# Optimization experiments

Measured on AMD Instinct MI355X. Metric: run time of the kernel, lower is better.

Reference implementation:

```python
import jax, jax.numpy as jnp
import numpy as np

N_NODES = 250000


def _gat_conv(x, src, dst, W, att_src, att_dst, bias, n_nodes):
    # PyG GATConv, heads=1, concat=True, negative_slope=0.2, self-loops already appended.
    h = x @ W                              # [N, 2]
    a_s = h @ att_src                      # [N]
    a_d = h @ att_dst                      # [N]
    e = jax.nn.leaky_relu(a_s[src] + a_d[dst], 0.2)   # [E]
    # segment softmax over incoming edges of each dst node
    m = jax.ops.segment_max(e, dst, num_segments=n_nodes)
    e = jnp.exp(e - m[dst])
    denom = jax.ops.segment_sum(e, dst, num_segments=n_nodes)
    alpha = e / (denom[dst] + 1e-16)       # [E]
    out = jax.ops.segment_sum(alpha[:, None] * h[src], dst, num_segments=n_nodes)
    return out + bias


def setup_inputs() -> dict:
    key = jax.random.key(0)
    ks = jax.random.split(key, 10)
    N, E = N_NODES, 16000000
    x = jax.random.normal(ks[0], (N, 4), dtype=jnp.float32)
    edge_index = jax.random.randint(ks[1], (2, E), 0, N, dtype=jnp.int64)
    def gat_params(k):
        k1, k2, k3 = jax.random.split(k, 3)
        return (jax.random.normal(k1, (2, 2), dtype=jnp.float32),
                jax.random.normal(k2, (2,), dtype=jnp.float32),
                jax.random.normal(k3, (2,), dtype=jnp.float32),
                jnp.zeros((2,), dtype=jnp.float32))
    W1, as1, ad1, b1 = gat_params(ks[2])
    W2, as2, ad2, b2 = gat_params(ks[3])
    return {"x": x, "edge_index": edge_index,
            "W_F1": W1, "att_src_F1": as1, "att_dst_F1": ad1, "bias_F1": b1,
            "W_F2": W2, "att_src_F2": as2, "att_dst_F2": ad2, "bias_F2": b2}


def reference(x, edge_index, W_F1, att_src_F1, att_dst_F1, bias_F1,
              W_F2, att_src_F2, att_dst_F2, bias_F2):
    n = x.shape[0]
    loop = jnp.arange(n, dtype=edge_index.dtype)
    src = jnp.concatenate([edge_index[0], loop])
    dst = jnp.concatenate([edge_index[1], loop])
    x1, x2 = x[:, :2], x[:, 2:]
    s_x = _gat_conv(x1, src, dst, W_F1, att_src_F1, att_dst_F1, bias_F1, n)
    t_x = _gat_conv(x1, src, dst, W_F2, att_src_F2, att_dst_F2, bias_F2, n)
    x1_new = x2 * jnp.exp(s_x) + t_x
    log_det = jnp.sum(s_x, axis=1)
    return (x1_new, x2, log_det)
```

## Files before the change

### kernel.cpp

```cpp
#include <hip/hip_runtime.h>


#define BSH 8
#define BSZ 256
#define NB  977
#define CAP 17408
#define EPB 32768
#define P1T 1024
#define P2T 1024
#define MPT 17

typedef int  iv4 __attribute__((ext_vector_type(4)));
typedef _Float16 h4 __attribute__((ext_vector_type(4)));

static __device__ __forceinline__ float lrelu(float z) { return z > 0.f ? z : 0.2f * z; }

__global__ void __launch_bounds__(P1T) bin_kernel(
    const int* __restrict__ ei, int E,
    const float* __restrict__ x, int N,
    const float* __restrict__ W1, const float* __restrict__ as1, const float* __restrict__ ad1,
    const float* __restrict__ W2, const float* __restrict__ as2, const float* __restrict__ ad2,
    h4* __restrict__ nodeSh, float4* __restrict__ nodeD,
    unsigned* __restrict__ bins, unsigned* __restrict__ cursor)
{
    __shared__ unsigned sorted[EPB];
    __shared__ unsigned lhist[NB];
    __shared__ unsigned lbase[NB];
    __shared__ unsigned sbase[NB + 1];
    __shared__ unsigned swv[16];

    int tid = threadIdx.x;

    {
        int i = blockIdx.x * 512 + (tid & 511);
        if (tid < 512 && i < N) {
            float4 xv = ((const float4*)x)[i];
            float x0 = xv.x, x1v = xv.y;
            float cs1_0 = W1[0] * as1[0] + W1[1] * as1[1];
            float cs1_1 = W1[2] * as1[0] + W1[3] * as1[1];
            float cd1_0 = W1[0] * ad1[0] + W1[1] * ad1[1];
            float cd1_1 = W1[2] * ad1[0] + W1[3] * ad1[1];
            float cs2_0 = W2[0] * as2[0] + W2[1] * as2[1];
            float cs2_1 = W2[2] * as2[0] + W2[3] * as2[1];
            float cd2_0 = W2[0] * ad2[0] + W2[1] * ad2[1];
            float cd2_1 = W2[2] * ad2[0] + W2[3] * ad2[1];
            nodeSh[i] = (h4){ (_Float16)x0, (_Float16)x1v,
                              (_Float16)(x0 * cs1_0 + x1v * cs1_1),
                              (_Float16)(x0 * cs2_0 + x1v * cs2_1) };
            nodeD[i] = make_float4(x0 * cd1_0 + x1v * cd1_1, x0 * cd2_0 + x1v * cd2_1,
                                   xv.z, xv.w);
        }
    }

    for (int i = tid; i < NB; i += P1T) lhist[i] = 0u;
    __syncthreads();

    const iv4* s4 = (const iv4*)ei;
    const iv4* d4 = (const iv4*)(ei + E);
    long long vbase = ((long long)blockIdx.x * EPB) >> 2;

    iv4 dv[8];
#pragma unroll
    for (int j = 0; j < 8; ++j) {
        long long v = vbase + (long long)j * P1T + tid;
        if (v * 4 < (long long)E) dv[j] = __builtin_nontemporal_load(&d4[v]);
        else dv[j] = (iv4){-1, -1, -1, -1};
    }
    unsigned rkp[16];
#pragma unroll
    for (int j = 0; j < 8; ++j) {
        int dd[4] = { dv[j].x, dv[j].y, dv[j].z, dv[j].w };
#pragma unroll
        for (int k = 0; k < 4; ++k) {
            unsigned r = 0;
            if (dd[k] >= 0) r = atomicAdd(&lhist[((unsigned)dd[k]) >> BSH], 1u);
            int idx = j * 4 + k;
            if (idx & 1) rkp[idx >> 1] |= (r << 16);
            else         rkp[idx >> 1] = r;
        }
    }
    __syncthreads();

    {
        unsigned v = (tid < NB) ? lhist[tid] : 0u;
        unsigned lane = (unsigned)tid & 63u;
        unsigned inc = v;
#pragma unroll
        for (int off = 1; off < 64; off <<= 1) {
            unsigned u = __shfl_up(inc, off, 64);
            if (lane >= (unsigned)off) inc += u;
        }
        if (lane == 63u) swv[tid >> 6] = inc;
        __syncthreads();
        if (tid == 0) {
            unsigned s = 0;
            sbase[0] = 0;
#pragma unroll
            for (int w = 0; w < 16; ++w) { unsigned t = swv[w]; swv[w] = s; s += t; }
        }
        __syncthreads();
        if (tid < NB) {
            sbase[tid + 1] = inc + swv[tid >> 6];
            unsigned c = lhist[tid];
            if (c) lbase[tid] = (unsigned)tid * CAP + atomicAdd(&cursor[tid], c);
        }
    }
    __syncthreads();

    iv4 sv[8];
#pragma unroll
    for (int j = 0; j < 8; ++j) {
        long long v = vbase + (long long)j * P1T + tid;
        if (v * 4 < (long long)E) sv[j] = __builtin_nontemporal_load(&s4[v]);
        else sv[j] = (iv4){0, 0, 0, 0};
    }
#pragma unroll
    for (int j = 0; j < 8; ++j) {
        int ss[4] = { sv[j].x, sv[j].y, sv[j].z, sv[j].w };
        int dd[4] = { dv[j].x, dv[j].y, dv[j].z, dv[j].w };
#pragma unroll
        for (int k = 0; k < 4; ++k) {
            if (dd[k] >= 0) {
                unsigned b = ((unsigned)dd[k]) >> BSH;
                int idx = j * 4 + k;
                unsigned r = (idx & 1) ? (rkp[idx >> 1] >> 16) : (rkp[idx >> 1] & 0xFFFFu);
                sorted[sbase[b] + r] = ((unsigned)ss[k] << BSH) | ((unsigned)dd[k] & (BSZ - 1u));
            }
        }
    }
    __syncthreads();

    int wid = tid >> 6;
    unsigned lane = (unsigned)tid & 63u;
    for (int b = wid; b < NB; b += 16) {
        unsigned L  = lhist[b];
        unsigned gb = lbase[b];
        unsigned sb = sbase[b];
        unsigned room = ((unsigned)b + 1u) * CAP - gb;
        if (L > room) L = room;
        for (unsigned off = lane; off < L; off += 64u)
            bins[gb + off] = sorted[sb + off];
    }
}

__global__ void __launch_bounds__(P2T) reduce_kernel(
    const unsigned* __restrict__ bins, const unsigned* __restrict__ cursor,
    const h4* __restrict__ nodeSh, const float4* __restrict__ nodeD, int N,
    const float* __restrict__ W1, const float* __restrict__ b1,
    const float* __restrict__ W2, const float* __restrict__ b2,
    float* __restrict__ out)
{
    __shared__ unsigned sorted[CAP];
    __shared__ unsigned hist[BSZ];
    __shared__ unsigned sbase[BSZ + 1];
    __shared__ unsigned swv[BSZ / 64];
    __shared__ float4   sD[BSZ];

    int b = blockIdx.x, tid = threadIdx.x;
    int node0 = b << BSH;
    unsigned start = (unsigned)b * CAP;
    unsigned cnt = cursor[b];
    if (cnt > CAP) cnt = CAP;

    if (tid < BSZ) {
        hist[tid] = 0u;
        int n = node0 + tid;
        sD[tid] = (n < N) ? nodeD[n] : make_float4(0.f, 0.f, 0.f, 0.f);
    }
    __syncthreads();

    unsigned ev[MPT];
#pragma unroll
    for (int j = 0; j < MPT; ++j) {
        unsigned i = (unsigned)tid + (unsigned)j * P2T;
        ev[j] = (i < cnt) ? __builtin_nontemporal_load(&bins[start + i]) : 0xFFFFFFFFu;
    }
    unsigned rkp[(MPT + 1) / 2];
#pragma unroll
    for (int j = 0; j < MPT; ++j) {
        unsigned r = 0;
        if (ev[j] != 0xFFFFFFFFu) r = atomicAdd(&hist[ev[j] & (BSZ - 1u)], 1u);
        if (j & 1) rkp[j >> 1] |= (r << 16);
        else       rkp[j >> 1] = r;
    }
    __syncthreads();

    if (tid < BSZ) {
        unsigned v = hist[tid];
        unsigned lane = (unsigned)tid & 63u;
#pragma unroll
        for (int off = 1; off < 64; off <<= 1) {
            unsigned u = __shfl_up(v, off, 64);
            if (lane >= (unsigned)off) v += u;
        }
        if (lane == 63u) swv[tid >> 6] = v;
        sbase[tid + 1] = v;
    }
    __syncthreads();
    if (tid == 0) {
        unsigned s = 0;
        sbase[0] = 0;
#pragma unroll
        for (int w = 0; w < BSZ / 64; ++w) { unsigned t = swv[w]; swv[w] = s; s += t; }
    }
    __syncthreads();
    if (tid < BSZ) sbase[tid + 1] += swv[tid >> 6];
    __syncthreads();

#pragma unroll
    for (int j = 0; j < MPT; ++j) {
        if (ev[j] != 0xFFFFFFFFu) {
            unsigned r = (j & 1) ? (rkp[j >> 1] >> 16) : (rkp[j >> 1] & 0xFFFFu);
            sorted[sbase[ev[j] & (BSZ - 1u)] + r] = ev[j];
        }
    }
    __syncthreads();

    int ln = tid >> 2;
    int q  = tid & 3;
    int n = node0 + ln;
    float4 Dv = sD[ln];
    float a0 = 0.f, a1 = 0.f, a2 = 0.f, a3 = 0.f, a4 = 0.f, a5 = 0.f;
    if (n < N) {
        unsigned beg = sbase[ln], end = sbase[ln + 1];
        unsigned i = beg + (unsigned)q;
        for (; i + 12u < end; i += 16u) {
            unsigned e0 = sorted[i];
            unsigned e1 = sorted[i + 4u];
            unsigned e2 = sorted[i + 8u];
            unsigned e3 = sorted[i + 12u];
            h4 S0 = nodeSh[e0 >> BSH];
            h4 S1 = nodeSh[e1 >> BSH];
            h4 S2 = nodeSh[e2 >> BSH];
            h4 S3 = nodeSh[e3 >> BSH];
            float w;
            w = __expf(lrelu((float)S0.z + Dv.x)); a0 += w * (float)S0.x; a1 += w * (float)S0.y; a2 += w;
            w = __expf(lrelu((float)S0.w + Dv.y)); a3 += w * (float)S0.x; a4 += w * (float)S0.y; a5 += w;
            w = __expf(lrelu((float)S1.z + Dv.x)); a0 += w * (float)S1.x; a1 += w * (float)S1.y; a2 += w;
            w = __expf(lrelu((float)S1.w + Dv.y)); a3 += w * (float)S1.x; a4 += w * (float)S1.y; a5 += w;
            w = __expf(lrelu((float)S2.z + Dv.x)); a0 += w * (float)S2.x; a1 += w * (float)S2.y; a2 += w;
            w = __expf(lrelu((float)S2.w + Dv.y)); a3 += w * (float)S2.x; a4 += w * (float)S2.y; a5 += w;
            w = __expf(lrelu((float)S3.z + Dv.x)); a0 += w * (float)S3.x; a1 += w * (float)S3.y; a2 += w;
            w = __expf(lrelu((float)S3.w + Dv.y)); a3 += w * (float)S3.x; a4 += w * (float)S3.y; a5 += w;
        }
        for (; i < end; i += 4u) {
            unsigned e = sorted[i];
            h4 S = nodeSh[e >> BSH];
            float w1 = __expf(lrelu((float)S.z + Dv.x));
            float w2 = __expf(lrelu((float)S.w + Dv.y));
            float sx = (float)S.x, sy = (float)S.y;
            a0 += w1 * sx; a1 += w1 * sy; a2 += w1;
            a3 += w2 * sx; a4 += w2 * sy; a5 += w2;
        }
    }
    a0 += __shfl_xor(a0, 1); a0 += __shfl_xor(a0, 2);
    a1 += __shfl_xor(a1, 1); a1 += __shfl_xor(a1, 2);
    a2 += __shfl_xor(a2, 1); a2 += __shfl_xor(a2, 2);
    a3 += __shfl_xor(a3, 1); a3 += __shfl_xor(a3, 2);
    a4 += __shfl_xor(a4, 1); a4 += __shfl_xor(a4, 2);
    a5 += __shfl_xor(a5, 1); a5 += __shfl_xor(a5, 2);
    if (q == 0 && n < N) {
        h4 S = nodeSh[n];
        float w1s = __expf(lrelu((float)S.z + Dv.x));
        float w2s = __expf(lrelu((float)S.w + Dv.y));
        float n1x = a0 + w1s * (float)S.x;
        float n1y = a1 + w1s * (float)S.y;
        float d1  = a2 + w1s + 1e-16f;
        float n2x = a3 + w2s * (float)S.x;
        float n2y = a4 + w2s * (float)S.y;
        float d2  = a5 + w2s + 1e-16f;
        float inv1 = 1.0f / d1, inv2 = 1.0f / d2;
        float s0 = (n1x * W1[0] + n1y * W1[2]) * inv1 + b1[0];
        float s1 = (n1x * W1[1] + n1y * W1[3]) * inv1 + b1[1];
        float t0 = (n2x * W2[0] + n2y * W2[2]) * inv2 + b2[0];
        float t1 = (n2x * W2[1] + n2y * W2[3]) * inv2 + b2[1];
        float x2a = Dv.z, x2b = Dv.w;
        out[2 * n]             = x2a * __expf(s0) + t0;
        out[2 * n + 1]         = x2b * __expf(s1) + t1;
        out[2 * N + 2 * n]     = x2a;
        out[2 * N + 2 * n + 1] = x2b;
        out[4 * N + n]         = s0 + s1;
    }
}

__global__ void __launch_bounds__(256) prep_kernel(
    const float* __restrict__ x, int N,
    const float* __restrict__ W1, const float* __restrict__ as1, const float* __restrict__ ad1,
    const float* __restrict__ W2, const float* __restrict__ as2, const float* __restrict__ ad2,
    h4* __restrict__ nodeSh, float4* __restrict__ nodeD, float* __restrict__ acc)
{
    int i = blockIdx.x * blockDim.x + threadIdx.x;
    if (i >= N) return;
    float4 xv = ((const float4*)x)[i];
    float x0 = xv.x, x1v = xv.y;
    float cs1_0 = W1[0] * as1[0] + W1[1] * as1[1];
    float cs1_1 = W1[2] * as1[0] + W1[3] * as1[1];
    float cd1_0 = W1[0] * ad1[0] + W1[1] * ad1[1];
    float cd1_1 = W1[2] * ad1[0] + W1[3] * ad1[1];
    float cs2_0 = W2[0] * as2[0] + W2[1] * as2[1];
    float cs2_1 = W2[2] * as2[0] + W2[3] * as2[1];
    float cd2_0 = W2[0] * ad2[0] + W2[1] * ad2[1];
    float cd2_1 = W2[2] * ad2[0] + W2[3] * ad2[1];
    nodeSh[i] = (h4){ (_Float16)x0, (_Float16)x1v,
                      (_Float16)(x0 * cs1_0 + x1v * cs1_1),
                      (_Float16)(x0 * cs2_0 + x1v * cs2_1) };
    nodeD[i] = make_float4(x0 * cd1_0 + x1v * cd1_1, x0 * cd2_0 + x1v * cd2_1, xv.z, xv.w);
    acc[i] = 0.f; acc[N + i] = 0.f; acc[2 * N + i] = 0.f;
    acc[3 * N + i] = 0.f; acc[4 * N + i] = 0.f; acc[5 * N + i] = 0.f;
}

__global__ void __launch_bounds__(256) edge_kernel(
    const int* __restrict__ ei, int E, int N,
    const h4* __restrict__ nodeSh, const float4* __restrict__ nodeD,
    float* __restrict__ acc)
{
    int e = blockIdx.x * blockDim.x + threadIdx.x;
    if (e >= E) return;
    int s = ei[e];
    int d = ei[E + e];
    h4 S = nodeSh[s];
    float4 D = nodeD[d];
    float w1 = __expf(lrelu((float)S.z + D.x));
    float w2 = __expf(lrelu((float)S.w + D.y));
    unsafeAtomicAdd(&acc[d],         w1 * (float)S.x);
    unsafeAtomicAdd(&acc[N + d],     w1 * (float)S.y);
    unsafeAtomicAdd(&acc[2 * N + d], w1);
    unsafeAtomicAdd(&acc[3 * N + d], w2 * (float)S.x);
    unsafeAtomicAdd(&acc[4 * N + d], w2 * (float)S.y);
    unsafeAtomicAdd(&acc[5 * N + d], w2);
}

__global__ void __launch_bounds__(256) fin_kernel(
    int N,
    const float* __restrict__ W1, const float* __restrict__ b1,
    const float* __restrict__ W2, const float* __restrict__ b2,
    const h4* __restrict__ nodeSh, const float4* __restrict__ nodeD,
    const float* __restrict__ acc, float* __restrict__ out)
{
    int i = blockIdx.x * blockDim.x + threadIdx.x;
    if (i >= N) return;
    h4 S = nodeSh[i];
    float4 D = nodeD[i];
    float w1s = __expf(lrelu((float)S.z + D.x));
    float w2s = __expf(lrelu((float)S.w + D.y));
    float n1x = acc[i] + w1s * (float)S.x;
    float n1y = acc[N + i] + w1s * (float)S.y;
    float d1  = acc[2 * N + i] + w1s + 1e-16f;
    float n2x = acc[3 * N + i] + w2s * (float)S.x;
    float n2y = acc[4 * N + i] + w2s * (float)S.y;
    float d2  = acc[5 * N + i] + w2s + 1e-16f;
    float inv1 = 1.0f / d1, inv2 = 1.0f / d2;
    float s0 = (n1x * W1[0] + n1y * W1[2]) * inv1 + b1[0];
    float s1 = (n1x * W1[1] + n1y * W1[3]) * inv1 + b1[1];
    float t0 = (n2x * W2[0] + n2y * W2[2]) * inv2 + b2[0];
    float t1 = (n2x * W2[1] + n2y * W2[3]) * inv2 + b2[1];
    float x2a = D.z, x2b = D.w;
    out[2 * i]             = x2a * __expf(s0) + t0;
    out[2 * i + 1]         = x2b * __expf(s1) + t1;
    out[2 * N + 2 * i]     = x2a;
    out[2 * N + 2 * i + 1] = x2b;
    out[4 * N + i]         = s0 + s1;
}

extern "C" void kernel_launch(void* const* d_in, const int* in_sizes, int n_in,
                              void* d_out, int out_size, void* d_ws, size_t ws_size,
                              hipStream_t stream)
{
    const float* x   = (const float*)d_in[0];
    const int*   ei  = (const int*)d_in[1];
    const float* W1  = (const float*)d_in[2];
    const float* as1 = (const float*)d_in[3];
    const float* ad1 = (const float*)d_in[4];
    const float* b1  = (const float*)d_in[5];
    const float* W2  = (const float*)d_in[6];
    const float* as2 = (const float*)d_in[7];
    const float* ad2 = (const float*)d_in[8];
    const float* b2  = (const float*)d_in[9];

    int N = in_sizes[0] / 4;
    int E = in_sizes[1] / 2;

    char* ws = (char*)d_ws;
    h4*       nodeSh = (h4*)ws;
    float4*   nodeD  = (float4*)(ws + (size_t)8 * N);
    size_t    off_c  = ((size_t)24 * N + 255) & ~(size_t)255;
    unsigned* cursor = (unsigned*)(ws + off_c);
    size_t    off_b  = (off_c + 4 * NB + 255) & ~(size_t)255;
    unsigned* bins   = (unsigned*)(ws + off_b);
    float*    acc    = (float*)(ws + off_b);
    float*    out    = (float*)d_out;

    size_t need = off_b + (size_t)4 * NB * CAP;
    int gb = (E + EPB - 1) / EPB;

    if (ws_size >= need && (E % 4) == 0 && (size_t)gb * 512 >= (size_t)N) {
        hipMemsetAsync(cursor, 0, sizeof(unsigned) * NB, stream);
        bin_kernel<<<gb, P1T, 0, stream>>>(ei, E, x, N, W1, as1, ad1, W2, as2, ad2,
                                           nodeSh, nodeD, bins, cursor);
        reduce_kernel<<<NB, P2T, 0, stream>>>(bins, cursor, nodeSh, nodeD, N,
                                              W1, b1, W2, b2, out);
    } else {
        int nb = (N + 255) / 256;
        prep_kernel<<<nb, 256, 0, stream>>>(x, N, W1, as1, ad1, W2, as2, ad2,
                                            nodeSh, nodeD, acc);
        int eb = (E + 255) / 256;
        edge_kernel<<<eb, 256, 0, stream>>>(ei, E, N, nodeSh, nodeD, acc);
        fin_kernel<<<nb, 256, 0, stream>>>(N, W1, b1, W2, b2, nodeSh, nodeD, acc, out);
    }
}
```

Before: 316.2 us.

## Pack bin cursors into 64-bit atomics, hoist src loads, vectorize bin reads

```diff
diff --git a/kernel.cpp b/kernel.cpp
--- a/kernel.cpp
+++ b/kernel.cpp
@@ -4,6 +4,7 @@
 #define BSH 8
 #define BSZ 256
 #define NB  977
+#define NBP4 245
 #define CAP 17408
 #define EPB 32768
 #define P1T 1024
@@ -21,7 +22,7 @@
     const float* __restrict__ W1, const float* __restrict__ as1, const float* __restrict__ ad1,
     const float* __restrict__ W2, const float* __restrict__ as2, const float* __restrict__ ad2,
     h4* __restrict__ nodeSh, float4* __restrict__ nodeD,
-    unsigned* __restrict__ bins, unsigned* __restrict__ cursor)
+    unsigned* __restrict__ bins, unsigned long long* __restrict__ cursor)
 {
     __shared__ unsigned sorted[EPB];
     __shared__ unsigned lhist[NB];
@@ -59,13 +60,20 @@
     const iv4* d4 = (const iv4*)(ei + E);
     long long vbase = ((long long)blockIdx.x * EPB) >> 2;
 
-    iv4 dv[8];
+    iv4 dv[8], sv[8];
 #pragma unroll
     for (int j = 0; j < 8; ++j) {
         long long v = vbase + (long long)j * P1T + tid;
         if (v * 4 < (long long)E) dv[j] = __builtin_nontemporal_load(&d4[v]);
         else dv[j] = (iv4){-1, -1, -1, -1};
     }
+#pragma unroll
+    for (int j = 0; j < 8; ++j) {
+        long long v = vbase + (long long)j * P1T + tid;
+        if (v * 4 < (long long)E) sv[j] = __builtin_nontemporal_load(&s4[v]);
+        else sv[j] = (iv4){0, 0, 0, 0};
+    }
+
     unsigned rkp[16];
 #pragma unroll
     for (int j = 0; j < 8; ++j) {
@@ -99,21 +107,27 @@
             for (int w = 0; w < 16; ++w) { unsigned t = swv[w]; swv[w] = s; s += t; }
         }
         __syncthreads();
-        if (tid < NB) {
-            sbase[tid + 1] = inc + swv[tid >> 6];
-            unsigned c = lhist[tid];
-            if (c) lbase[tid] = (unsigned)tid * CAP + atomicAdd(&cursor[tid], c);
-        }
-    }
-    __syncthreads();
-
-    iv4 sv[8];
-#pragma unroll
-    for (int j = 0; j < 8; ++j) {
-        long long v = vbase + (long long)j * P1T + tid;
-        if (v * 4 < (long long)E) sv[j] = __builtin_nontemporal_load(&s4[v]);
-        else sv[j] = (iv4){0, 0, 0, 0};
-    }
+        if (tid < NB) sbase[tid + 1] = inc + swv[tid >> 6];
+        if (tid < NBP4) {
+            int b0 = tid * 4;
+            unsigned long long add = 0;
+#pragma unroll
+            for (int k = 0; k < 4; ++k) {
+                int bb = b0 + k;
+                unsigned c = (bb < NB) ? lhist[bb] : 0u;
+                add |= (unsigned long long)(c & 0xFFFFu) << (16 * k);
+            }
+            unsigned long long old = atomicAdd(&cursor[tid], add);
+#pragma unroll
+            for (int k = 0; k < 4; ++k) {
+                int bb = b0 + k;
+                if (bb < NB)
+                    lbase[bb] = (unsigned)bb * CAP + (unsigned)((old >> (16 * k)) & 0xFFFFu);
+            }
+        }
+    }
+    __syncthreads();
+
 #pragma unroll
     for (int j = 0; j < 8; ++j) {
         int ss[4] = { sv[j].x, sv[j].y, sv[j].z, sv[j].w };
@@ -144,7 +158,7 @@
 }
 
 __global__ void __launch_bounds__(P2T) reduce_kernel(
-    const unsigned* __restrict__ bins, const unsigned* __restrict__ cursor,
+    const unsigned* __restrict__ bins, const unsigned long long* __restrict__ cursor,
     const h4* __restrict__ nodeSh, const float4* __restrict__ nodeD, int N,
     const float* __restrict__ W1, const float* __restrict__ b1,
     const float* __restrict__ W2, const float* __restrict__ b2,
@@ -159,7 +173,7 @@
     int b = blockIdx.x, tid = threadIdx.x;
     int node0 = b << BSH;
     unsigned start = (unsigned)b * CAP;
-    unsigned cnt = cursor[b];
+    unsigned cnt = ((const unsigned short*)cursor)[b];
     if (cnt > CAP) cnt = CAP;
 
     if (tid < BSZ) {
@@ -170,10 +184,24 @@
     __syncthreads();
 
     unsigned ev[MPT];
-#pragma unroll
-    for (int j = 0; j < MPT; ++j) {
-        unsigned i = (unsigned)tid + (unsigned)j * P2T;
-        ev[j] = (i < cnt) ? __builtin_nontemporal_load(&bins[start + i]) : 0xFFFFFFFFu;
+    {
+        const iv4* b4 = (const iv4*)(bins + start);
+#pragma unroll
+        for (int j = 0; j < 4; ++j) {
+            unsigned g = (unsigned)tid + (unsigned)j * P2T;
+            unsigned p = 4u * g;
+            if (p + 3u < cnt) {
+                iv4 v = __builtin_nontemporal_load(&b4[g]);
+                ev[4 * j + 0] = (unsigned)v.x; ev[4 * j + 1] = (unsigned)v.y;
+                ev[4 * j + 2] = (unsigned)v.z; ev[4 * j + 3] = (unsigned)v.w;
+            } else {
+#pragma unroll
+                for (int k = 0; k < 4; ++k)
+                    ev[4 * j + k] = (p + (unsigned)k < cnt) ? bins[start + p + k] : 0xFFFFFFFFu;
+            }
+        }
+        unsigned p = 16u * P2T + (unsigned)tid;
+        ev[16] = (p < cnt) ? bins[start + p] : 0xFFFFFFFFu;
     }
     unsigned rkp[(MPT + 1) / 2];
 #pragma unroll
@@ -384,8 +412,8 @@
     h4*       nodeSh = (h4*)ws;
     float4*   nodeD  = (float4*)(ws + (size_t)8 * N);
     size_t    off_c  = ((size_t)24 * N + 255) & ~(size_t)255;
-    unsigned* cursor = (unsigned*)(ws + off_c);
-    size_t    off_b  = (off_c + 4 * NB + 255) & ~(size_t)255;
+    unsigned long long* cursor = (unsigned long long*)(ws + off_c);
+    size_t    off_b  = (off_c + 8 * NBP4 + 255) & ~(size_t)255;
     unsigned* bins   = (unsigned*)(ws + off_b);
     float*    acc    = (float*)(ws + off_b);
     float*    out    = (float*)d_out;
@@ -394,7 +422,7 @@
     int gb = (E + EPB - 1) / EPB;
 
     if (ws_size >= need && (E % 4) == 0 && (size_t)gb * 512 >= (size_t)N) {
-        hipMemsetAsync(cursor, 0, sizeof(unsigned) * NB, stream);
+        hipMemsetAsync(cursor, 0, sizeof(unsigned long long) * NBP4, stream);
         bin_kernel<<<gb, P1T, 0, stream>>>(ei, E, x, N, W1, as1, ad1, W2, as2, ad2,
                                            nodeSh, nodeD, bins, cursor);
         reduce_kernel<<<NB, P2T, 0, stream>>>(bins, cursor, nodeSh, nodeD, N,
```

Measured after the change: 318.1 us. About the same (+0.6%).
